# Optimization experiments

Measured on AMD Instinct MI355X. Metric: run time of the kernel, lower is better.

The kernel has to match this reference:

```python
import jax, jax.numpy as jnp
import numpy as np

DIM = 256
TIME_DIM = 64
BETA = 0.5
VOCAB = 150
B, L = 2048, 128


def setup_inputs() -> dict:
    key = jax.random.key(0)
    ks = jax.random.split(key, 9)
    u = lambda k, shape: jax.random.uniform(k, shape, jnp.float32, -0.1, 0.1)
    return {
        "out": jax.random.normal(ks[0], (B, L, DIM), jnp.float32),
        "hn": jax.random.normal(ks[1], (B, DIM), jnp.float32),
        "pos_ind": jax.random.randint(ks[2], (B, L), 0, VOCAB),
        "rel_dt": jax.random.randint(ks[3], (B, L), 0, VOCAB),
        "abs_dt": jnp.zeros((B, L), jnp.float32),
        "pos_emb_w": u(ks[4], (VOCAB, TIME_DIM)),
        "rel_emb_w": u(ks[5], (VOCAB, TIME_DIM)),
        "Wk": u(ks[6], (DIM, DIM)),   # fc_k.weight: y = x @ Wk.T
        "Wq": u(ks[7], (DIM, DIM)),   # fc_q.weight
        "Wrp": u(ks[8], (1, 2 * TIME_DIM)),  # fc_rp.weight
    }


def reference(out, hn, pos_ind, rel_dt, abs_dt, pos_emb_w, rel_emb_w, Wk, Wq, Wrp):
    temperature = np.sqrt(DIM * 1.0).astype(np.float32)
    pad_mask = pos_ind == 0                      # [B, L]
    pos_e = pos_emb_w[pos_ind]                   # [B, L, T]
    rel_e = rel_emb_w[rel_dt]                    # [B, L, T]
    attn_k = jnp.einsum('bld,ed->ble', out, Wk)  # fc_k(out)
    attn_q = jnp.einsum('bd,ed->be', hn, Wq)     # fc_q(hn)
    attn_0 = jnp.einsum('bld,bd->bl', attn_k, attn_q) / temperature
    attn_1 = jnp.einsum('blt,ot->bl', jnp.concatenate([rel_e, pos_e], -1), Wrp)
    attn = attn_0 + BETA * attn_1
    attn = jnp.where(pad_mask, -jnp.inf, attn)
    attn = jax.nn.softmax(attn, axis=1)
    return jnp.einsum('bl,bld->bd', attn, out)   # [B, D]
```

## Files before the change

kernel.cpp:

```cpp
#include <hip/hip_runtime.h>

#define DIM 256
#define L_ 128
#define TD 64
#define NVOCAB 150
#define NB 2048

__global__ __launch_bounds__(256) void prep_kernel(
    const float* __restrict__ Wk, const float* __restrict__ Wq,
    const float* __restrict__ Wrp,
    const float* __restrict__ rel_emb_w, const float* __restrict__ pos_emb_w,
    float* __restrict__ M, float* __restrict__ rel_s, float* __restrict__ pos_s)
{
    if (blockIdx.x == DIM) {
        int v = threadIdx.x;
        if (v < NVOCAB) {
            float sr = 0.f, sp = 0.f;
#pragma unroll 8
            for (int j = 0; j < TD; ++j) {
                sr = fmaf(rel_emb_w[v * TD + j], Wrp[j], sr);
                sp = fmaf(pos_emb_w[v * TD + j], Wrp[TD + j], sp);
            }
            rel_s[v] = 0.5f * sr;
            pos_s[v] = 0.5f * sp;
        }
        return;
    }
    int cc = blockIdx.x;
    int d  = threadIdx.x;
    float acc = 0.f;
#pragma unroll 8
    for (int e = 0; e < DIM; ++e)
        acc = fmaf(Wq[e * DIM + cc], Wk[e * DIM + d], acc);
    M[cc * DIM + d] = acc * (1.0f / 16.0f);
}

__global__ __launch_bounds__(256) void qk_bias_kernel(
    const float* __restrict__ hn, const float* __restrict__ M,
    const int* __restrict__ pos_ind, const int* __restrict__ rel_dt,
    const float* __restrict__ rel_s, const float* __restrict__ pos_s,
    float* __restrict__ qk, float* __restrict__ bias_g)
{
    const int t = threadIdx.x;
    if (blockIdx.x >= NB / 8) {
        int idx = (blockIdx.x - NB / 8) * 256 + t;
        int pi = pos_ind[idx];
        int rd = rel_dt[idx];
        bias_g[idx] = (pi == 0) ? -1e30f : (rel_s[rd] + pos_s[pi]);
        return;
    }
    __shared__ float hn_s[8][DIM];
    const int r0 = blockIdx.x * 8;
#pragma unroll
    for (int i = 0; i < 8; ++i)
        hn_s[i][t] = hn[(size_t)(r0 + i) * DIM + t];
    __syncthreads();
    float acc[8] = {0.f, 0.f, 0.f, 0.f, 0.f, 0.f, 0.f, 0.f};
#pragma unroll 8
    for (int c = 0; c < DIM; ++c) {
        float m = M[c * DIM + t];
#pragma unroll
        for (int r = 0; r < 8; ++r)
            acc[r] = fmaf(hn_s[r][c], m, acc[r]);
    }
#pragma unroll
    for (int r = 0; r < 8; ++r)
        qk[(size_t)(r0 + r) * DIM + t] = acc[r];
}

__device__ __forceinline__ float dot4(float4 a, float4 b) {
    return fmaf(a.x, b.x, fmaf(a.y, b.y, fmaf(a.z, b.z, a.w * b.w)));
}

__global__ __launch_bounds__(512, 4) void attn_main(
    const float* __restrict__ outp, const float* __restrict__ qk,
    const float* __restrict__ bias_g, float* __restrict__ y)
{
    const int b    = blockIdx.x;
    const int t    = threadIdx.x;
    const int w    = t >> 6;
    const int lane = t & 63;
    const int g    = lane >> 4;
    const int c    = lane & 15;
    const int grp  = (w << 2) | g;

    __shared__ float mG[32];
    __shared__ float dG[32];
    __shared__ float red[32][DIM];

    const float4* __restrict__ src = (const float4*)outp + (size_t)b * (L_ * 64);
    const int r0   = (w << 4) | g;
    const int base = r0 * 64 + c;

    float4 v[16];
#pragma unroll
    for (int k = 0; k < 4; ++k)
#pragma unroll
        for (int j = 0; j < 4; ++j)
            v[k * 4 + j] = src[base + k * 256 + j * 16];

    const float4* __restrict__ qp = (const float4*)qk + (size_t)b * 64;
    float4 q[4];
#pragma unroll
    for (int j = 0; j < 4; ++j) q[j] = qp[c + j * 16];
    const float* __restrict__ bp = bias_g + (size_t)b * L_ + r0;
    float bi[4];
#pragma unroll
    for (int k = 0; k < 4; ++k) bi[k] = bp[4 * k];

    float lg[4];
#pragma unroll
    for (int k = 0; k < 4; ++k) {
        float p = dot4(v[k * 4 + 0], q[0]) + dot4(v[k * 4 + 1], q[1]) +
                  dot4(v[k * 4 + 2], q[2]) + dot4(v[k * 4 + 3], q[3]);
        p += __shfl_xor(p, 1);
        p += __shfl_xor(p, 2);
        p += __shfl_xor(p, 4);
        p += __shfl_xor(p, 8);
        lg[k] = p + bi[k];
    }

    const float m = fmaxf(fmaxf(lg[0], lg[1]), fmaxf(lg[2], lg[3]));
    float we[4];
    float d = 0.f;
#pragma unroll
    for (int k = 0; k < 4; ++k) { we[k] = __expf(lg[k] - m); d += we[k]; }

    float4 o[4];
#pragma unroll
    for (int j = 0; j < 4; ++j) o[j] = make_float4(0.f, 0.f, 0.f, 0.f);
#pragma unroll
    for (int k = 0; k < 4; ++k)
#pragma unroll
        for (int j = 0; j < 4; ++j) {
            o[j].x = fmaf(we[k], v[k * 4 + j].x, o[j].x);
            o[j].y = fmaf(we[k], v[k * 4 + j].y, o[j].y);
            o[j].z = fmaf(we[k], v[k * 4 + j].z, o[j].z);
            o[j].w = fmaf(we[k], v[k * 4 + j].w, o[j].w);
        }

    if (c == 0) { mG[grp] = m; dG[grp] = d; }
    __syncthreads();

    float Mx = -1e30f;
#pragma unroll
    for (int i = 0; i < 32; ++i) Mx = fmaxf(Mx, mG[i]);
    float term = (lane < 32) ? __expf(mG[lane] - Mx) * dG[lane] : 0.f;
#pragma unroll
    for (int off = 32; off >= 1; off >>= 1) term += __shfl_xor(term, off, 64);
    const float f = __expf(m - Mx) / term;

    float4* rw = (float4*)(&red[grp][0]);
#pragma unroll
    for (int j = 0; j < 4; ++j)
        rw[c + j * 16] = make_float4(o[j].x * f, o[j].y * f, o[j].z * f, o[j].w * f);
    __syncthreads();

    if (t < DIM) {
        float s = 0.f;
#pragma unroll
        for (int gg = 0; gg < 32; ++gg) s += red[gg][t];
        y[(size_t)b * DIM + t] = s;
    }
}

extern "C" void kernel_launch(void* const* d_in, const int* in_sizes, int n_in,
                              void* d_out, int out_size, void* d_ws, size_t ws_size,
                              hipStream_t stream)
{
    const float* out_t     = (const float*)d_in[0];
    const float* hn        = (const float*)d_in[1];
    const int*   pos_ind   = (const int*)  d_in[2];
    const int*   rel_dt    = (const int*)  d_in[3];
    const float* pos_emb_w = (const float*)d_in[5];
    const float* rel_emb_w = (const float*)d_in[6];
    const float* Wk        = (const float*)d_in[7];
    const float* Wq        = (const float*)d_in[8];
    const float* Wrp       = (const float*)d_in[9];

    float* y = (float*)d_out;

    float* M      = (float*)d_ws;
    float* qk     = M + DIM * DIM;
    float* rel_s  = qk + (size_t)NB * DIM;
    float* pos_s  = rel_s + 256;
    float* bias_g = pos_s + 256;

    prep_kernel<<<DIM + 1, 256, 0, stream>>>(Wk, Wq, Wrp, rel_emb_w, pos_emb_w,
                                             M, rel_s, pos_s);
    qk_bias_kernel<<<NB / 8 + (NB * L_) / 256, 256, 0, stream>>>(
        hn, M, pos_ind, rel_dt, rel_s, pos_s, qk, bias_g);
    attn_main<<<NB, 512, 0, stream>>>(out_t, qk, bias_g, y);
}
```

Measured before the change: 70.79 us.

## Fuse bias gather into attention kernel and drop softmax max pass

```diff
diff --git a/kernel.cpp b/kernel.cpp
--- a/kernel.cpp
+++ b/kernel.cpp
@@ -5,6 +5,10 @@
 #define TD 64
 #define NVOCAB 150
 #define NB 2048
+
+__device__ __forceinline__ float dot4(float4 a, float4 b) {
+    return fmaf(a.x, b.x, fmaf(a.y, b.y, fmaf(a.z, b.z, a.w * b.w)));
+}
 
 __global__ __launch_bounds__(256) void prep_kernel(
     const float* __restrict__ Wk, const float* __restrict__ Wq,
@@ -28,29 +32,24 @@
     }
     int cc = blockIdx.x;
     int d  = threadIdx.x;
-    float acc = 0.f;
+    float a0 = 0.f, a1 = 0.f, a2 = 0.f, a3 = 0.f;
 #pragma unroll 8
-    for (int e = 0; e < DIM; ++e)
-        acc = fmaf(Wq[e * DIM + cc], Wk[e * DIM + d], acc);
-    M[cc * DIM + d] = acc * (1.0f / 16.0f);
+    for (int e = 0; e < DIM; e += 4) {
+        a0 = fmaf(Wq[(e + 0) * DIM + cc], Wk[(e + 0) * DIM + d], a0);
+        a1 = fmaf(Wq[(e + 1) * DIM + cc], Wk[(e + 1) * DIM + d], a1);
+        a2 = fmaf(Wq[(e + 2) * DIM + cc], Wk[(e + 2) * DIM + d], a2);
+        a3 = fmaf(Wq[(e + 3) * DIM + cc], Wk[(e + 3) * DIM + d], a3);
+    }
+    M[cc * DIM + d] = (a0 + a1 + a2 + a3) * (1.0f / 16.0f);
 }
 
-__global__ __launch_bounds__(256) void qk_bias_kernel(
+__global__ __launch_bounds__(256) void qk_kernel(
     const float* __restrict__ hn, const float* __restrict__ M,
-    const int* __restrict__ pos_ind, const int* __restrict__ rel_dt,
-    const float* __restrict__ rel_s, const float* __restrict__ pos_s,
-    float* __restrict__ qk, float* __restrict__ bias_g)
+    float* __restrict__ qk)
 {
-    const int t = threadIdx.x;
-    if (blockIdx.x >= NB / 8) {
-        int idx = (blockIdx.x - NB / 8) * 256 + t;
-        int pi = pos_ind[idx];
-        int rd = rel_dt[idx];
-        bias_g[idx] = (pi == 0) ? -1e30f : (rel_s[rd] + pos_s[pi]);
-        return;
-    }
     __shared__ float hn_s[8][DIM];
     const int r0 = blockIdx.x * 8;
+    const int t = threadIdx.x;
 #pragma unroll
     for (int i = 0; i < 8; ++i)
         hn_s[i][t] = hn[(size_t)(r0 + i) * DIM + t];
@@ -68,13 +67,11 @@
         qk[(size_t)(r0 + r) * DIM + t] = acc[r];
 }
 
-__device__ __forceinline__ float dot4(float4 a, float4 b) {
-    return fmaf(a.x, b.x, fmaf(a.y, b.y, fmaf(a.z, b.z, a.w * b.w)));
-}
-
 __global__ __launch_bounds__(512, 4) void attn_main(
     const float* __restrict__ outp, const float* __restrict__ qk,
-    const float* __restrict__ bias_g, float* __restrict__ y)
+    const int* __restrict__ pos_ind, const int* __restrict__ rel_dt,
+    const float* __restrict__ rel_s, const float* __restrict__ pos_s,
+    float* __restrict__ y)
 {
     const int b    = blockIdx.x;
     const int t    = threadIdx.x;
@@ -82,16 +79,13 @@
     const int lane = t & 63;
     const int g    = lane >> 4;
     const int c    = lane & 15;
-    const int grp  = (w << 2) | g;
 
-    __shared__ float mG[32];
-    __shared__ float dG[32];
-    __shared__ float red[32][DIM];
+    __shared__ float red[8][DIM];
+    __shared__ float dW[8];
 
     const float4* __restrict__ src = (const float4*)outp + (size_t)b * (L_ * 64);
     const int r0   = (w << 4) | g;
     const int base = r0 * 64 + c;
-
     float4 v[16];
 #pragma unroll
     for (int k = 0; k < 4; ++k)
@@ -102,11 +96,16 @@
     const float4* __restrict__ qp = (const float4*)qk + (size_t)b * 64;
     float4 q[4];
 #pragma unroll
-    for (int j = 0; j < 4; ++j) q[j] = qp[c + j * 16];
-    const float* __restrict__ bp = bias_g + (size_t)b * L_ + r0;
+    for (int j = 0; j < 4; ++j) q[j] = qp[j * 16 + c];
+
     float bi[4];
 #pragma unroll
-    for (int k = 0; k < 4; ++k) bi[k] = bp[4 * k];
+    for (int k = 0; k < 4; ++k) {
+        int row = r0 + 4 * k;
+        int pi = pos_ind[b * L_ + row];
+        int rd = rel_dt[b * L_ + row];
+        bi[k] = (pi == 0) ? -1e30f : (rel_s[rd] + pos_s[pi]);
+    }
 
     float lg[4];
 #pragma unroll
@@ -120,11 +119,10 @@
         lg[k] = p + bi[k];
     }
 
-    const float m = fmaxf(fmaxf(lg[0], lg[1]), fmaxf(lg[2], lg[3]));
     float we[4];
     float d = 0.f;
 #pragma unroll
-    for (int k = 0; k < 4; ++k) { we[k] = __expf(lg[k] - m); d += we[k]; }
+    for (int k = 0; k < 4; ++k) { we[k] = __expf(lg[k]); d += we[k]; }
 
     float4 o[4];
 #pragma unroll
@@ -139,28 +137,29 @@
             o[j].w = fmaf(we[k], v[k * 4 + j].w, o[j].w);
         }
 
-    if (c == 0) { mG[grp] = m; dG[grp] = d; }
-    __syncthreads();
+#pragma unroll
+    for (int j = 0; j < 4; ++j) {
+        o[j].x += __shfl_xor(o[j].x, 16); o[j].y += __shfl_xor(o[j].y, 16);
+        o[j].z += __shfl_xor(o[j].z, 16); o[j].w += __shfl_xor(o[j].w, 16);
+        o[j].x += __shfl_xor(o[j].x, 32); o[j].y += __shfl_xor(o[j].y, 32);
+        o[j].z += __shfl_xor(o[j].z, 32); o[j].w += __shfl_xor(o[j].w, 32);
+    }
+    d += __shfl_xor(d, 16);
+    d += __shfl_xor(d, 32);
 
-    float Mx = -1e30f;
+    if (g == 0) {
+        float4* rw = (float4*)(&red[w][0]);
 #pragma unroll
-    for (int i = 0; i < 32; ++i) Mx = fmaxf(Mx, mG[i]);
-    float term = (lane < 32) ? __expf(mG[lane] - Mx) * dG[lane] : 0.f;
-#pragma unroll
-    for (int off = 32; off >= 1; off >>= 1) term += __shfl_xor(term, off, 64);
-    const float f = __expf(m - Mx) / term;
-
-    float4* rw = (float4*)(&red[grp][0]);
-#pragma unroll
-    for (int j = 0; j < 4; ++j)
-        rw[c + j * 16] = make_float4(o[j].x * f, o[j].y * f, o[j].z * f, o[j].w * f);
+        for (int j = 0; j < 4; ++j) rw[j * 16 + c] = o[j];
+        if (lane == 0) dW[w] = d;
+    }
     __syncthreads();
 
     if (t < DIM) {
-        float s = 0.f;
+        float s = 0.f, D = 0.f;
 #pragma unroll
-        for (int gg = 0; gg < 32; ++gg) s += red[gg][t];
-        y[(size_t)b * DIM + t] = s;
+        for (int ww = 0; ww < 8; ++ww) { s += red[ww][t]; D += dW[ww]; }
+        y[(size_t)b * DIM + t] = s / D;
     }
 }
 
@@ -180,15 +179,14 @@
 
     float* y = (float*)d_out;
 
-    float* M      = (float*)d_ws;
-    float* qk     = M + DIM * DIM;
-    float* rel_s  = qk + (size_t)NB * DIM;
-    float* pos_s  = rel_s + 256;
-    float* bias_g = pos_s + 256;
+    float* M     = (float*)d_ws;
+    float* qk    = M + DIM * DIM;
+    float* rel_s = qk + (size_t)NB * DIM;
+    float* pos_s = rel_s + 256;
 
     prep_kernel<<<DIM + 1, 256, 0, stream>>>(Wk, Wq, Wrp, rel_emb_w, pos_emb_w,
                                              M, rel_s, pos_s);
-    qk_bias_kernel<<<NB / 8 + (NB * L_) / 256, 256, 0, stream>>>(
-        hn, M, pos_ind, rel_dt, rel_s, pos_s, qk, bias_g);
-    attn_main<<<NB, 512, 0, stream>>>(out_t, qk, bias_g, y);
+    qk_kernel<<<NB / 8, 256, 0, stream>>>(hn, M, qk);
+    attn_main<<<NB, 512, 0, stream>>>(out_t, qk, pos_ind, rel_dt,
+                                      rel_s, pos_s, y);
 }
```

Measured after the change: 86.26 us. 1.22x slower.
